# Optimization experiments

Hardware: AMD Instinct MI355X
Metric: run time of the kernel (lower is better)

## Reference

```python
import jax, jax.numpy as jnp
import numpy as np

HEAD_DIM = 1024
SCALE = HEAD_DIM ** -0.25  # qk_scale defaults to exponent -0.25


def setup_inputs() -> dict:
    key = jax.random.key(0)
    ks = jax.random.split(key, 6)
    B_s, B_q, C = 4096, 4096, 1024
    return {
        "query": jax.random.normal(ks[0], (B_q, C), dtype=jnp.float32),
        "s": jax.random.normal(ks[1], (B_s, C), dtype=jnp.float32),
        "TG_prompt": jax.random.normal(ks[2], (B_s, C), dtype=jnp.float32),
        "W_qkv": jax.random.normal(ks[3], (3 * HEAD_DIM, C), dtype=jnp.float32) * (C ** -0.5),
        "W_proj_s": jax.random.normal(ks[4], (HEAD_DIM, HEAD_DIM), dtype=jnp.float32) * (HEAD_DIM ** -0.5),
        "W_proj_q": jax.random.normal(ks[5], (HEAD_DIM, HEAD_DIM), dtype=jnp.float32) * (HEAD_DIM ** -0.5),
    }


def reference(query, s, TG_prompt, W_qkv, W_proj_s, W_proj_q):
    B_s = s.shape[0]
    t = s + TG_prompt                       # [B_s, C]
    c = jnp.concatenate([t, query], axis=0)  # [B, C], B = B_s + B_q
    x = c @ W_qkv.T                          # [B, 3*head_dim]
    q, k, v = jnp.split(x, 3, axis=-1)       # each [B, head_dim]
    # separate sqrt-scale on q and k, then full [B, B] scores
    attn = jax.nn.softmax((q * SCALE) @ (k.T * SCALE), axis=-1)
    attn_cq = attn[:B_s, B_s:]               # [B_s, B_q]
    attn_qc = attn[B_s:, :B_s]               # [B_q, B_s]
    # matmul against raw query / s (NOT v), then per-branch projection
    x_s = (attn_cq @ query) @ W_proj_s.T     # [B_s, head_dim]
    x_q = (attn_qc @ s) @ W_proj_q.T         # [B_q, head_dim]
    return (x_s, x_q)
```

## Files before the change

kernel.cpp:

```cpp
#include <hip/hip_runtime.h>


typedef unsigned short u16;
typedef __bf16 bf16x8 __attribute__((ext_vector_type(8)));
typedef float f32x4 __attribute__((ext_vector_type(4)));
typedef unsigned short u16x8 __attribute__((ext_vector_type(8)));

#define DEVI static __device__ __forceinline__

DEVI u16 f2b(float f) {
  unsigned int u = __float_as_uint(f);
  u += 0x7fffu + ((u >> 16) & 1u);
  return (u16)(u >> 16);
}

DEVI float exp2_hw(float x) {
  float r;
  asm("v_exp_f32 %0, %1" : "=v"(r) : "v"(x));
  return r;
}


__global__ void prep_c(const float* __restrict__ query, const float* __restrict__ s,
                       const float* __restrict__ tg, u16* __restrict__ cB) {
  int base = (blockIdx.x * 256 + threadIdx.x) << 3;
  int row = base >> 10;
  u16x8 o;
  if (row < 4096) {
    float4 a0 = *(const float4*)(s + base);
    float4 a1 = *(const float4*)(s + base + 4);
    float4 b0 = *(const float4*)(tg + base);
    float4 b1 = *(const float4*)(tg + base + 4);
    o[0] = f2b(a0.x + b0.x); o[1] = f2b(a0.y + b0.y);
    o[2] = f2b(a0.z + b0.z); o[3] = f2b(a0.w + b0.w);
    o[4] = f2b(a1.x + b1.x); o[5] = f2b(a1.y + b1.y);
    o[6] = f2b(a1.z + b1.z); o[7] = f2b(a1.w + b1.w);
  } else {
    int qb = base - 4096 * 1024;
    float4 a0 = *(const float4*)(query + qb);
    float4 a1 = *(const float4*)(query + qb + 4);
    o[0] = f2b(a0.x); o[1] = f2b(a0.y); o[2] = f2b(a0.z); o[3] = f2b(a0.w);
    o[4] = f2b(a1.x); o[5] = f2b(a1.y); o[6] = f2b(a1.z); o[7] = f2b(a1.w);
  }
  *(u16x8*)(cB + base) = o;
}

__global__ void conv3(const float* __restrict__ w0, const float* __restrict__ w1,
                      const float* __restrict__ w2, u16* __restrict__ o0,
                      u16* __restrict__ o1, u16* __restrict__ o2) {
  int b = blockIdx.x;
  const float* in; u16* out; int lb;
  if (b < 1024)      { in = w0; out = o0; lb = b; }
  else if (b < 1536) { in = w1; out = o1; lb = b - 1024; }
  else               { in = w2; out = o2; lb = b - 1536; }
  int base = (lb * 256 + threadIdx.x) << 3;
  float4 a0 = *(const float4*)(in + base);
  float4 a1 = *(const float4*)(in + base + 4);
  u16x8 o;
  o[0] = f2b(a0.x); o[1] = f2b(a0.y); o[2] = f2b(a0.z); o[3] = f2b(a0.w);
  o[4] = f2b(a1.x); o[5] = f2b(a1.y); o[6] = f2b(a1.z); o[7] = f2b(a1.w);
  *(u16x8*)(out + base) = o;
}

__global__ void transpose2(const float* __restrict__ query, const float* __restrict__ s,
                           u16* __restrict__ queryT, u16* __restrict__ sT) {
  __shared__ float tile[32][33];
  const float* in = blockIdx.z ? s : query;
  u16* out = blockIdx.z ? sT : queryT;
  int c0 = blockIdx.x * 32, r0 = blockIdx.y * 32;
  int tx = threadIdx.x, ty = threadIdx.y;
#pragma unroll
  for (int i = 0; i < 4; ++i)
    tile[ty + i * 8][tx] = in[(size_t)(r0 + ty + i * 8) * 1024 + c0 + tx];
  __syncthreads();
#pragma unroll
  for (int i = 0; i < 4; ++i)
    out[(size_t)(c0 + ty + i * 8) * 4096 + r0 + tx] = f2b(tile[tx][ty + i * 8]);
}


template <int EPI>
__global__ __launch_bounds__(256)
void gemm_bt(const u16* __restrict__ A, const u16* __restrict__ A1,
             const u16* __restrict__ B, const u16* __restrict__ B1,
             int lda, int ldb, int K, int ldc,
             u16* __restrict__ outb, u16* __restrict__ outb1,
             float* __restrict__ outf, float* __restrict__ outf1,
             float sq, float sk,
             const float* __restrict__ rs, const float* __restrict__ rs1,
             u16* __restrict__ Pcq, u16* __restrict__ Pqc,
             float* __restrict__ rowsum) {
  __shared__ __align__(16) u16 sA[128 * 64];
  __shared__ __align__(16) u16 sB[128 * 64];
  const int tid = threadIdx.x;
  const int lane = tid & 63;
  const int wave = tid >> 6;
  const int wr = (wave >> 1) * 64;
  const int wc = (wave & 1) * 64;
  const int ar = lane & 15;
  const int by = blockIdx.y, bx = blockIdx.x;
  const int z = (EPI == 2 || EPI == 3) ? blockIdx.z : 0;

  const u16* Ab = (z ? A1 : A) + (size_t)(by * 128) * lda;
  const u16* Bb = (z ? B1 : B) + (size_t)(bx * 128) * ldb;

  f32x4 zero = {0.0f, 0.0f, 0.0f, 0.0f};
  f32x4 acc[4][4];
#pragma unroll
  for (int i = 0; i < 4; ++i)
#pragma unroll
    for (int j = 0; j < 4; ++j) acc[i][j] = zero;

  const int sr = tid >> 3;
  const int scL = (tid & 7) << 3;
  const int scG = ((tid & 7) ^ (sr & 7)) << 3;

  const int l7 = lane & 7, l16 = lane >> 4;
  const int p0b = (l16 ^ l7) << 4;
  const int offA0 = (wr + ar) * 128 + p0b;
  const int offB0 = (wc + ar) * 128 + p0b;
  const char* sAc = (const char*)sA;
  const char* sBc = (const char*)sB;

  for (int k0 = 0; k0 < K; k0 += 64) {
#pragma unroll
    for (int it = 0; it < 4; ++it) {
      int r = it * 32 + sr;
      __builtin_amdgcn_global_load_lds(
          (__attribute__((address_space(1))) void*)(Ab + (size_t)r * lda + k0 + scG),
          (__attribute__((address_space(3))) void*)(sA + r * 64 + scL), 16, 0, 0);
    }
#pragma unroll
    for (int it = 0; it < 4; ++it) {
      int r = it * 32 + sr;
      __builtin_amdgcn_global_load_lds(
          (__attribute__((address_space(1))) void*)(Bb + (size_t)r * ldb + k0 + scG),
          (__attribute__((address_space(3))) void*)(sB + r * 64 + scL), 16, 0, 0);
    }
    __syncthreads();
#pragma unroll
    for (int half = 0; half < 2; ++half) {
      const int px = half ? 64 : 0;
      bf16x8 af[4], bfr[4];
#pragma unroll
      for (int t = 0; t < 4; ++t)
        af[t] = *(const bf16x8*)(sAc + ((offA0 ^ px) + t * 2048));
#pragma unroll
      for (int t = 0; t < 4; ++t)
        bfr[t] = *(const bf16x8*)(sBc + ((offB0 ^ px) + t * 2048));
#pragma unroll
      for (int tm = 0; tm < 4; ++tm)
#pragma unroll
        for (int tn = 0; tn < 4; ++tn)
          acc[tm][tn] = __builtin_amdgcn_mfma_f32_16x16x32_bf16(
              af[tm], bfr[tn], acc[tm][tn], 0, 0, 0);
    }
    __syncthreads();
  }

  const int qr = (lane >> 4) * 4;
  const int qc = lane & 15;

  if constexpr (EPI == 0) {
#pragma unroll
    for (int tm = 0; tm < 4; ++tm)
#pragma unroll
      for (int r = 0; r < 4; ++r) {
        int row = by * 128 + wr + tm * 16 + qr + r;
#pragma unroll
        for (int tn = 0; tn < 4; ++tn) {
          int col = bx * 128 + wc + tn * 16 + qc;
          float sc = (col < 1024) ? sq : sk;
          outb[(size_t)row * ldc + col] = f2b(acc[tm][tn][r] * sc);
        }
      }
  } else if constexpr (EPI == 1) {
    const bool top = (by < 32);
    const bool left = (bx < 32);
    u16* pdst = nullptr;
    if (top && !left) pdst = Pcq;
    if (!top && left) pdst = Pqc;
    const int rofs = top ? 0 : 4096;
    const int cofs = left ? 0 : 4096;
#pragma unroll
    for (int tm = 0; tm < 4; ++tm) {
      float rsum[4] = {0.f, 0.f, 0.f, 0.f};
#pragma unroll
      for (int tn = 0; tn < 4; ++tn) {
        float e[4];
#pragma unroll
        for (int r = 0; r < 4; ++r) {
          e[r] = exp2_hw(acc[tm][tn][r]);
          rsum[r] += e[r];
        }
        if (pdst) {
          int col = bx * 128 + wc + tn * 16 + qc - cofs;
#pragma unroll
          for (int r = 0; r < 4; ++r) {
            int row = by * 128 + wr + tm * 16 + qr + r - rofs;
            pdst[(size_t)row * 4096 + col] = f2b(e[r]);
          }
        }
      }
#pragma unroll
      for (int r = 0; r < 4; ++r) {
        float v = rsum[r];
        v += __shfl_xor(v, 1);
        v += __shfl_xor(v, 2);
        v += __shfl_xor(v, 4);
        v += __shfl_xor(v, 8);
        if ((lane & 15) == 0)
          atomicAdd(&rowsum[by * 128 + wr + tm * 16 + qr + r], v);
      }
    }
  } else if constexpr (EPI == 2) {
    u16* ob = z ? outb1 : outb;
    const float* rsz = z ? rs1 : rs;
#pragma unroll
    for (int tm = 0; tm < 4; ++tm)
#pragma unroll
      for (int r = 0; r < 4; ++r) {
        int row = by * 128 + wr + tm * 16 + qr + r;
        float inv = 1.0f / rsz[row];
#pragma unroll
        for (int tn = 0; tn < 4; ++tn) {
          int col = bx * 128 + wc + tn * 16 + qc;
          ob[(size_t)row * ldc + col] = f2b(acc[tm][tn][r] * inv);
        }
      }
  } else {
    float* of = z ? outf1 : outf;
#pragma unroll
    for (int tm = 0; tm < 4; ++tm)
#pragma unroll
      for (int r = 0; r < 4; ++r) {
        int row = by * 128 + wr + tm * 16 + qr + r;
#pragma unroll
        for (int tn = 0; tn < 4; ++tn) {
          int col = bx * 128 + wc + tn * 16 + qc;
          of[(size_t)row * ldc + col] = acc[tm][tn][r];
        }
      }
  }
}


extern "C" void kernel_launch(void* const* d_in, const int* in_sizes, int n_in,
                              void* d_out, int out_size, void* d_ws, size_t ws_size,
                              hipStream_t stream) {
  (void)in_sizes; (void)n_in; (void)out_size; (void)ws_size;
  const float* query = (const float*)d_in[0];
  const float* s     = (const float*)d_in[1];
  const float* tg    = (const float*)d_in[2];
  const float* Wqkv  = (const float*)d_in[3];
  const float* Wps   = (const float*)d_in[4];
  const float* Wpq   = (const float*)d_in[5];
  float* out = (float*)d_out;

  char* ws = (char*)d_ws;
  u16* cB     = (u16*)ws; ws += (size_t)8192 * 1024 * 2;
  u16* qks    = (u16*)ws; ws += (size_t)8192 * 2048 * 2;
  u16* queryT = (u16*)ws; ws += (size_t)1024 * 4096 * 2;
  u16* sT     = (u16*)ws; ws += (size_t)1024 * 4096 * 2;
  u16* WqkB   = (u16*)ws; ws += (size_t)2048 * 1024 * 2;
  u16* WpsB   = (u16*)ws; ws += (size_t)1024 * 1024 * 2;
  u16* WpqB   = (u16*)ws; ws += (size_t)1024 * 1024 * 2;
  u16* Pcq    = (u16*)ws; ws += (size_t)4096 * 4096 * 2;
  u16* Pqc    = (u16*)ws; ws += (size_t)4096 * 4096 * 2;
  u16* Ys     = (u16*)ws; ws += (size_t)4096 * 1024 * 2;
  u16* Yq     = (u16*)ws; ws += (size_t)4096 * 1024 * 2;
  float* rowsum = (float*)ws;

  const float SCALE = 0.17677669529663687f;
  const float LOG2E = 1.4426950408889634f;

  (void)hipMemsetAsync(rowsum, 0, 8192 * sizeof(float), stream);
  prep_c<<<4096, 256, 0, stream>>>(query, s, tg, cB);
  conv3<<<2048, 256, 0, stream>>>(Wqkv, Wps, Wpq, WqkB, WpsB, WpqB);
  transpose2<<<dim3(32, 128, 2), dim3(32, 8), 0, stream>>>(query, s, queryT, sT);

  gemm_bt<0><<<dim3(16, 64), 256, 0, stream>>>(
      cB, nullptr, WqkB, nullptr, 1024, 1024, 1024, 2048,
      qks, nullptr, nullptr, nullptr, SCALE * LOG2E, SCALE,
      nullptr, nullptr, nullptr, nullptr, nullptr);
  gemm_bt<1><<<dim3(64, 64), 256, 0, stream>>>(
      qks, nullptr, qks + 1024, nullptr, 2048, 2048, 1024, 0,
      nullptr, nullptr, nullptr, nullptr, 0.f, 0.f,
      nullptr, nullptr, Pcq, Pqc, rowsum);
  gemm_bt<2><<<dim3(8, 32, 2), 256, 0, stream>>>(
      Pcq, Pqc, queryT, sT, 4096, 4096, 4096, 1024,
      Ys, Yq, nullptr, nullptr, 0.f, 0.f,
      rowsum, rowsum + 4096, nullptr, nullptr, nullptr);
  gemm_bt<3><<<dim3(8, 32, 2), 256, 0, stream>>>(
      Ys, Yq, WpsB, WpqB, 1024, 1024, 1024, 1024,
      nullptr, nullptr, out, out + (size_t)4096 * 1024, 0.f, 0.f,
      nullptr, nullptr, nullptr, nullptr, nullptr);
}
```

Measured before the change: 479.4 us.

## Reassociate projection before attention, drop transpose kernel, stage P stores through LDS

Uses associativity to precompute W_proj·query^T and W_proj·s^T (VsT, VqT) as a small GEMM on bf16 copies of the inputs. The attention-times-V GEMM then writes the final fp32 output directly after row normalization. This removes the separate transpose kernel and the final projection GEMM along with its intermediate round trip. The softmax epilogue now stages exp tiles through shared memory so P is stored with 16-byte row-contiguous writes instead of scattered 2-byte stores. A bf16 copy of s is added in prep_c, and rounding moves to the projected V, which slightly changes numerics.

Result: faster. 458.2 us (-4.4%).

```diff
diff --git a/kernel.cpp b/kernel.cpp
--- a/kernel.cpp
+++ b/kernel.cpp
@@ -22,7 +22,8 @@
 
 
 __global__ void prep_c(const float* __restrict__ query, const float* __restrict__ s,
-                       const float* __restrict__ tg, u16* __restrict__ cB) {
+                       const float* __restrict__ tg, u16* __restrict__ cB,
+                       u16* __restrict__ sBf) {
   int base = (blockIdx.x * 256 + threadIdx.x) << 3;
   int row = base >> 10;
   u16x8 o;
@@ -31,6 +32,10 @@
     float4 a1 = *(const float4*)(s + base + 4);
     float4 b0 = *(const float4*)(tg + base);
     float4 b1 = *(const float4*)(tg + base + 4);
+    u16x8 os;
+    os[0] = f2b(a0.x); os[1] = f2b(a0.y); os[2] = f2b(a0.z); os[3] = f2b(a0.w);
+    os[4] = f2b(a1.x); os[5] = f2b(a1.y); os[6] = f2b(a1.z); os[7] = f2b(a1.w);
+    *(u16x8*)(sBf + base) = os;
     o[0] = f2b(a0.x + b0.x); o[1] = f2b(a0.y + b0.y);
     o[2] = f2b(a0.z + b0.z); o[3] = f2b(a0.w + b0.w);
     o[4] = f2b(a1.x + b1.x); o[5] = f2b(a1.y + b1.y);
@@ -60,22 +65,6 @@
   o[0] = f2b(a0.x); o[1] = f2b(a0.y); o[2] = f2b(a0.z); o[3] = f2b(a0.w);
   o[4] = f2b(a1.x); o[5] = f2b(a1.y); o[6] = f2b(a1.z); o[7] = f2b(a1.w);
   *(u16x8*)(out + base) = o;
-}
-
-__global__ void transpose2(const float* __restrict__ query, const float* __restrict__ s,
-                           u16* __restrict__ queryT, u16* __restrict__ sT) {
-  __shared__ float tile[32][33];
-  const float* in = blockIdx.z ? s : query;
-  u16* out = blockIdx.z ? sT : queryT;
-  int c0 = blockIdx.x * 32, r0 = blockIdx.y * 32;
-  int tx = threadIdx.x, ty = threadIdx.y;
-#pragma unroll
-  for (int i = 0; i < 4; ++i)
-    tile[ty + i * 8][tx] = in[(size_t)(r0 + ty + i * 8) * 1024 + c0 + tx];
-  __syncthreads();
-#pragma unroll
-  for (int i = 0; i < 4; ++i)
-    out[(size_t)(c0 + ty + i * 8) * 4096 + r0 + tx] = f2b(tile[tx][ty + i * 8]);
 }
 
 
@@ -99,7 +88,7 @@
   const int wc = (wave & 1) * 64;
   const int ar = lane & 15;
   const int by = blockIdx.y, bx = blockIdx.x;
-  const int z = (EPI == 2 || EPI == 3) ? blockIdx.z : 0;
+  const int z = blockIdx.z;
 
   const u16* Ab = (z ? A1 : A) + (size_t)(by * 128) * lda;
   const u16* Bb = (z ? B1 : B) + (size_t)(bx * 128) * ldb;
@@ -180,28 +169,21 @@
     u16* pdst = nullptr;
     if (top && !left) pdst = Pcq;
     if (!top && left) pdst = Pqc;
-    const int rofs = top ? 0 : 4096;
-    const int cofs = left ? 0 : 4096;
+    const int growb = by * 128 + wr;
+    const int rbase = growb - (top ? 0 : 4096);
+    const int cbase = bx * 128 + wc - (left ? 0 : 4096);
+    u16* wbuf = sA + wave * 1152;
 #pragma unroll
     for (int tm = 0; tm < 4; ++tm) {
+      float e[4][4];
       float rsum[4] = {0.f, 0.f, 0.f, 0.f};
 #pragma unroll
-      for (int tn = 0; tn < 4; ++tn) {
-        float e[4];
+      for (int tn = 0; tn < 4; ++tn)
 #pragma unroll
         for (int r = 0; r < 4; ++r) {
-          e[r] = exp2_hw(acc[tm][tn][r]);
-          rsum[r] += e[r];
-        }
-        if (pdst) {
-          int col = bx * 128 + wc + tn * 16 + qc - cofs;
-#pragma unroll
-          for (int r = 0; r < 4; ++r) {
-            int row = by * 128 + wr + tm * 16 + qr + r - rofs;
-            pdst[(size_t)row * 4096 + col] = f2b(e[r]);
-          }
-        }
-      }
+          e[tn][r] = exp2_hw(acc[tm][tn][r]);
+          rsum[r] += e[tn][r];
+        }
 #pragma unroll
       for (int r = 0; r < 4; ++r) {
         float v = rsum[r];
@@ -210,11 +192,27 @@
         v += __shfl_xor(v, 4);
         v += __shfl_xor(v, 8);
         if ((lane & 15) == 0)
-          atomicAdd(&rowsum[by * 128 + wr + tm * 16 + qr + r], v);
-      }
-    }
-  } else if constexpr (EPI == 2) {
-    u16* ob = z ? outb1 : outb;
+          atomicAdd(&rowsum[growb + tm * 16 + qr + r], v);
+      }
+      if (pdst) {
+#pragma unroll
+        for (int tn = 0; tn < 4; ++tn)
+#pragma unroll
+          for (int r = 0; r < 4; ++r)
+            wbuf[(qr + r) * 72 + tn * 16 + qc] = f2b(e[tn][r]);
+        asm volatile("" ::: "memory");
+#pragma unroll
+        for (int p = 0; p < 2; ++p) {
+          int lr = p * 8 + (lane >> 3);
+          int lc = (lane & 7) * 8;
+          bf16x8 vv = *(const bf16x8*)(wbuf + lr * 72 + lc);
+          *(bf16x8*)(pdst + (size_t)(rbase + tm * 16 + lr) * 4096 + cbase + lc) = vv;
+        }
+        asm volatile("" ::: "memory");
+      }
+    }
+  } else if constexpr (EPI == 4) {
+    float* of = z ? outf1 : outf;
     const float* rsz = z ? rs1 : rs;
 #pragma unroll
     for (int tm = 0; tm < 4; ++tm)
@@ -225,11 +223,11 @@
 #pragma unroll
         for (int tn = 0; tn < 4; ++tn) {
           int col = bx * 128 + wc + tn * 16 + qc;
-          ob[(size_t)row * ldc + col] = f2b(acc[tm][tn][r] * inv);
+          of[(size_t)row * ldc + col] = acc[tm][tn][r] * inv;
         }
       }
   } else {
-    float* of = z ? outf1 : outf;
+    u16* ob = z ? outb1 : outb;
 #pragma unroll
     for (int tm = 0; tm < 4; ++tm)
 #pragma unroll
@@ -238,7 +236,7 @@
 #pragma unroll
         for (int tn = 0; tn < 4; ++tn) {
           int col = bx * 128 + wc + tn * 16 + qc;
-          of[(size_t)row * ldc + col] = acc[tm][tn][r];
+          ob[(size_t)row * ldc + col] = f2b(acc[tm][tn][r]);
         }
       }
   }
@@ -259,26 +257,30 @@
 
   char* ws = (char*)d_ws;
   u16* cB     = (u16*)ws; ws += (size_t)8192 * 1024 * 2;
+  u16* sBf    = (u16*)ws; ws += (size_t)4096 * 1024 * 2;
   u16* qks    = (u16*)ws; ws += (size_t)8192 * 2048 * 2;
-  u16* queryT = (u16*)ws; ws += (size_t)1024 * 4096 * 2;
-  u16* sT     = (u16*)ws; ws += (size_t)1024 * 4096 * 2;
   u16* WqkB   = (u16*)ws; ws += (size_t)2048 * 1024 * 2;
   u16* WpsB   = (u16*)ws; ws += (size_t)1024 * 1024 * 2;
   u16* WpqB   = (u16*)ws; ws += (size_t)1024 * 1024 * 2;
+  u16* VsT    = (u16*)ws; ws += (size_t)1024 * 4096 * 2;
+  u16* VqT    = (u16*)ws; ws += (size_t)1024 * 4096 * 2;
   u16* Pcq    = (u16*)ws; ws += (size_t)4096 * 4096 * 2;
   u16* Pqc    = (u16*)ws; ws += (size_t)4096 * 4096 * 2;
-  u16* Ys     = (u16*)ws; ws += (size_t)4096 * 1024 * 2;
-  u16* Yq     = (u16*)ws; ws += (size_t)4096 * 1024 * 2;
   float* rowsum = (float*)ws;
+
+  const u16* qBf = cB + (size_t)4096 * 1024;
 
   const float SCALE = 0.17677669529663687f;
   const float LOG2E = 1.4426950408889634f;
 
   (void)hipMemsetAsync(rowsum, 0, 8192 * sizeof(float), stream);
-  prep_c<<<4096, 256, 0, stream>>>(query, s, tg, cB);
+  prep_c<<<4096, 256, 0, stream>>>(query, s, tg, cB, sBf);
   conv3<<<2048, 256, 0, stream>>>(Wqkv, Wps, Wpq, WqkB, WpsB, WpqB);
-  transpose2<<<dim3(32, 128, 2), dim3(32, 8), 0, stream>>>(query, s, queryT, sT);
-
+
+  gemm_bt<5><<<dim3(32, 8, 2), 256, 0, stream>>>(
+      WpsB, WpqB, qBf, sBf, 1024, 1024, 1024, 4096,
+      VsT, VqT, nullptr, nullptr, 0.f, 0.f,
+      nullptr, nullptr, nullptr, nullptr, nullptr);
   gemm_bt<0><<<dim3(16, 64), 256, 0, stream>>>(
       cB, nullptr, WqkB, nullptr, 1024, 1024, 1024, 2048,
       qks, nullptr, nullptr, nullptr, SCALE * LOG2E, SCALE,
@@ -287,12 +289,8 @@
       qks, nullptr, qks + 1024, nullptr, 2048, 2048, 1024, 0,
       nullptr, nullptr, nullptr, nullptr, 0.f, 0.f,
       nullptr, nullptr, Pcq, Pqc, rowsum);
-  gemm_bt<2><<<dim3(8, 32, 2), 256, 0, stream>>>(
-      Pcq, Pqc, queryT, sT, 4096, 4096, 4096, 1024,
-      Ys, Yq, nullptr, nullptr, 0.f, 0.f,
+  gemm_bt<4><<<dim3(8, 32, 2), 256, 0, stream>>>(
+      Pcq, Pqc, VsT, VqT, 4096, 4096, 4096, 1024,
+      nullptr, nullptr, out, out + (size_t)4096 * 1024, 0.f, 0.f,
       rowsum, rowsum + 4096, nullptr, nullptr, nullptr);
-  gemm_bt<3><<<dim3(8, 32, 2), 256, 0, stream>>>(
-      Ys, Yq, WpsB, WpqB, 1024, 1024, 1024, 1024,
-      nullptr, nullptr, out, out + (size_t)4096 * 1024, 0.f, 0.f,
-      nullptr, nullptr, nullptr, nullptr, nullptr);
-}
+}
```
